# Optimization experiments

Hardware: AMD Instinct MI355X
Metric: run time of the kernel (lower is better)

## Reference

```python
import jax, jax.numpy as jnp
import numpy as np
from jax.scipy.special import logsumexp

DIM_RHO = 128
DIM_C = 128
HID_F = 512   # hidden of MLP2 f
HID_F2 = 256  # hidden of MLP f2 (fixed 128->256->128 in source)
B, S, N = 64, 2048, 100000


def setup_inputs() -> dict:
    key = jax.random.key(0)
    ks = jax.random.split(key, 16)
    def lin(k, fan_in, fan_out):
        bound = 1.0 / np.sqrt(fan_in)
        kw, kb = jax.random.split(k)
        W = jax.random.uniform(kw, (fan_in, fan_out), jnp.float32, -bound, bound)
        b = jax.random.uniform(kb, (fan_out,), jnp.float32, -bound, bound)
        return W, b
    rho = jax.random.normal(ks[0], (B, S, DIM_RHO), jnp.float32)
    c = jax.random.normal(ks[1], (N, DIM_C), jnp.float32)
    w = jax.random.uniform(ks[2], (B, S), jnp.float32, 0.1, 1.0)
    l = jax.random.uniform(ks[3], (B,), jnp.float32, 0.1, 1.0)
    roads = jax.random.randint(ks[4], (B, S), 0, N + 1)  # 0 = pad row
    f2_W1, f2_b1 = lin(ks[5], DIM_C, HID_F2)
    f2_W2, f2_b2 = lin(ks[6], HID_F2, DIM_C)
    f_W1, f_b1 = lin(ks[7], DIM_RHO + DIM_C, HID_F)
    f_W21, f_b21 = lin(ks[8], HID_F, 1)
    f_W22, f_b22 = lin(ks[9], HID_F, 1)
    return {"rho": rho, "c": c, "w": w, "l": l, "roads": roads,
            "f2_W1": f2_W1, "f2_b1": f2_b1, "f2_W2": f2_W2, "f2_b2": f2_b2,
            "f_W1": f_W1, "f_b1": f_b1, "f_W21": f_W21, "f_b21": f_b21,
            "f_W22": f_W22, "f_b22": f_b22}


def reference(rho, c, w, l, roads, f2_W1, f2_b1, f2_W2, f2_b2,
              f_W1, f_b1, f_W21, f_b21, f_W22, f_b22):
    # pad row 0 with zeros, gather per-edge node features: (B, S, dim_c)
    c_padded = jnp.concatenate([jnp.zeros((1, c.shape[1]), c.dtype), c], axis=0)
    c_stack = c_padded[roads]
    # f2: MLP with SELU (dropout inactive at eval)
    h2 = jax.nn.selu(jnp.einsum('bsd,dh->bsh', c_stack, f2_W1) + f2_b1)
    c_t = jnp.einsum('bsh,hd->bsd', h2, f2_W2) + f2_b2
    # f: MLP2 with ReLU (use_selu=False), two heads
    x = jnp.concatenate([rho, c_t], axis=2)  # (B, S, 256)
    h1 = jax.nn.relu(jnp.einsum('bsd,dh->bsh', x, f_W1) + f_b1)
    logm = (jnp.einsum('bsh,ho->bso', h1, f_W21) + f_b21)[..., 0]  # (B, S)
    logv = (jnp.einsum('bsh,ho->bso', h1, f_W22) + f_b22)[..., 0]
    logw = jnp.log(w)
    logm_agg = logsumexp(logm + logw, axis=1)
    logv_agg = logsumexp(logv + 2.0 * logw, axis=1)
    logl = jnp.log(l)
    log_mu = logl - logm_agg
    log_lam = logl - 3.0 * logm_agg - logv_agg
    return (log_mu, log_lam)
```

## Files before the change

kernel.cpp:

```cpp
#include <hip/hip_runtime.h>
#include <hip/hip_bf16.h>

typedef __attribute__((ext_vector_type(8))) short short8;
typedef __attribute__((ext_vector_type(4))) float f32x4;

__device__ __forceinline__ unsigned short f2bf(float f){
    unsigned u = __float_as_uint(f);
    unsigned r = (u + 0x7FFFu + ((u >> 16) & 1u)) >> 16;
    return (unsigned short)r;
}

__device__ __forceinline__ unsigned swz(unsigned row, unsigned byte_in_row, unsigned stride){
    return (row * stride + byte_in_row) ^ ((row & 7u) << 4);
}

__global__ void prep_weights(const float* __restrict__ W1, const float* __restrict__ W2,
                             const float* __restrict__ W3,
                             unsigned short* __restrict__ W1T,
                             unsigned short* __restrict__ W2T,
                             unsigned short* __restrict__ W3T){
    int i = blockIdx.x * 256 + threadIdx.x;
    if (i < 32768){
        int n = i >> 7, k = i & 127;
        W1T[i] = f2bf(W1[k * 256 + n]);
    } else if (i < 65536){
        int j = i - 32768; int n = j >> 8, k = j & 255;
        W2T[j] = f2bf(W2[k * 128 + n]);
    } else if (i < 196608){
        int j = i - 65536; int n = j >> 8, k = j & 255;
        W3T[j] = f2bf(W3[k * 512 + n]);
    }
}

__launch_bounds__(256, 2)
__global__ void main_kernel(const float* __restrict__ rho,
                            const float* __restrict__ c,
                            const float* __restrict__ w,
                            const int*  __restrict__ roads,
                            const unsigned short* __restrict__ W1T,
                            const float* __restrict__ b1,
                            const unsigned short* __restrict__ W2T,
                            const float* __restrict__ b2,
                            const unsigned short* __restrict__ W3T,
                            const float* __restrict__ b3,
                            const float* __restrict__ w21,
                            const float* __restrict__ b21s,
                            const float* __restrict__ w22,
                            const float* __restrict__ b22s,
                            float* __restrict__ pm,
                            float* __restrict__ pv)
{
    __shared__ __align__(16) unsigned char smem[81920];
    unsigned char* sXc = smem;
    unsigned char* sH2 = smem + 16384;
    unsigned char* sX  = smem + 49152;
    float* sPm = (float*)smem;
    float* sPv = (float*)(smem + 4096);

    const int tid = threadIdx.x;
    const int t0  = blockIdx.x * 64;

    for (int u = tid; u < 64 * 32; u += 256){
        int row = u >> 5, ch = u & 31;
        int road = roads[t0 + row];
        float4 v = make_float4(0.f, 0.f, 0.f, 0.f);
        if (road > 0)
            v = reinterpret_cast<const float4*>(c + (size_t)(road - 1) * 128)[ch];
        ushort4 h;
        h.x = f2bf(v.x); h.y = f2bf(v.y); h.z = f2bf(v.z); h.w = f2bf(v.w);
        *reinterpret_cast<ushort4*>(sXc + swz(row, ch * 8, 256)) = h;

        float4 rv = reinterpret_cast<const float4*>(rho + (size_t)(t0 + row) * 128)[ch];
        ushort4 rh;
        rh.x = f2bf(rv.x); rh.y = f2bf(rv.y); rh.z = f2bf(rv.z); rh.w = f2bf(rv.w);
        *reinterpret_cast<ushort4*>(sX + swz(row, ch * 8, 512)) = rh;
    }
    __syncthreads();

    const int lane = tid & 63, wv = tid >> 6;
    const int lr = lane & 15, lg = lane >> 4;

    #pragma unroll
    for (int nc = 0; nc < 4; ++nc){
        const int n = wv * 64 + nc * 16 + lr;
        short8 b[4];
        #pragma unroll
        for (int kk = 0; kk < 4; ++kk)
            b[kk] = *reinterpret_cast<const short8*>(W1T + n * 128 + kk * 32 + lg * 8);
        f32x4 acc[4] = {{0.f,0.f,0.f,0.f},{0.f,0.f,0.f,0.f},{0.f,0.f,0.f,0.f},{0.f,0.f,0.f,0.f}};
        #pragma unroll
        for (int kk = 0; kk < 4; ++kk){
            #pragma unroll
            for (int mt = 0; mt < 4; ++mt){
                short8 a = *reinterpret_cast<const short8*>(sXc + swz(mt * 16 + lr, kk * 64 + lg * 16, 256));
                acc[mt] = __builtin_amdgcn_mfma_f32_16x16x32_bf16(a, b[kk], acc[mt], 0, 0, 0);
            }
        }
        float bias = b1[n];
        #pragma unroll
        for (int mt = 0; mt < 4; ++mt){
            #pragma unroll
            for (int r = 0; r < 4; ++r){
                float vv = acc[mt][r] + bias;
                vv = (vv > 0.f) ? 1.0507009873554805f * vv
                                : 1.7580993408473766f * expm1f(vv);
                *reinterpret_cast<unsigned short*>(sH2 + swz(mt * 16 + lg * 4 + r, n * 2, 512)) = f2bf(vv);
            }
        }
    }
    __syncthreads();

    #pragma unroll
    for (int nc = 0; nc < 2; ++nc){
        const int n = wv * 32 + nc * 16 + lr;
        short8 b[8];
        #pragma unroll
        for (int kk = 0; kk < 8; ++kk)
            b[kk] = *reinterpret_cast<const short8*>(W2T + n * 256 + kk * 32 + lg * 8);
        f32x4 acc[4] = {{0.f,0.f,0.f,0.f},{0.f,0.f,0.f,0.f},{0.f,0.f,0.f,0.f},{0.f,0.f,0.f,0.f}};
        #pragma unroll
        for (int kk = 0; kk < 8; ++kk){
            #pragma unroll
            for (int mt = 0; mt < 4; ++mt){
                short8 a = *reinterpret_cast<const short8*>(sH2 + swz(mt * 16 + lr, kk * 64 + lg * 16, 512));
                acc[mt] = __builtin_amdgcn_mfma_f32_16x16x32_bf16(a, b[kk], acc[mt], 0, 0, 0);
            }
        }
        float bias = b2[n];
        #pragma unroll
        for (int mt = 0; mt < 4; ++mt){
            #pragma unroll
            for (int r = 0; r < 4; ++r){
                float vv = acc[mt][r] + bias;
                *reinterpret_cast<unsigned short*>(sX + swz(mt * 16 + lg * 4 + r, (128 + n) * 2, 512)) = f2bf(vv);
            }
        }
    }
    __syncthreads();

    float hm[4][4] = {};
    float hv[4][4] = {};
    #pragma unroll 2
    for (int nc = 0; nc < 8; ++nc){
        const int n = wv * 128 + nc * 16 + lr;
        short8 b[8];
        #pragma unroll
        for (int kk = 0; kk < 8; ++kk)
            b[kk] = *reinterpret_cast<const short8*>(W3T + n * 256 + kk * 32 + lg * 8);
        f32x4 acc[4] = {{0.f,0.f,0.f,0.f},{0.f,0.f,0.f,0.f},{0.f,0.f,0.f,0.f},{0.f,0.f,0.f,0.f}};
        #pragma unroll
        for (int kk = 0; kk < 8; ++kk){
            #pragma unroll
            for (int mt = 0; mt < 4; ++mt){
                short8 a = *reinterpret_cast<const short8*>(sX + swz(mt * 16 + lr, kk * 64 + lg * 16, 512));
                acc[mt] = __builtin_amdgcn_mfma_f32_16x16x32_bf16(a, b[kk], acc[mt], 0, 0, 0);
            }
        }
        float bias = b3[n];
        float wm = w21[n], wvv = w22[n];
        #pragma unroll
        for (int mt = 0; mt < 4; ++mt){
            #pragma unroll
            for (int r = 0; r < 4; ++r){
                float h = fmaxf(acc[mt][r] + bias, 0.f);
                hm[mt][r] += h * wm;
                hv[mt][r] += h * wvv;
            }
        }
    }
    #pragma unroll
    for (int off = 1; off < 16; off <<= 1){
        #pragma unroll
        for (int mt = 0; mt < 4; ++mt){
            #pragma unroll
            for (int r = 0; r < 4; ++r){
                hm[mt][r] += __shfl_xor(hm[mt][r], off, 64);
                hv[mt][r] += __shfl_xor(hv[mt][r], off, 64);
            }
        }
    }
    if (lr == 0){
        #pragma unroll
        for (int mt = 0; mt < 4; ++mt){
            #pragma unroll
            for (int r = 0; r < 4; ++r){
                int row = mt * 16 + lg * 4 + r;
                sPm[wv * 64 + row] = hm[mt][r];
                sPv[wv * 64 + row] = hv[mt][r];
            }
        }
    }
    __syncthreads();
    if (tid < 64){
        float B21 = b21s[0], B22 = b22s[0];
        float m_ = sPm[tid] + sPm[64 + tid] + sPm[128 + tid] + sPm[192 + tid] + B21;
        float v_ = sPv[tid] + sPv[64 + tid] + sPv[128 + tid] + sPv[192 + tid] + B22;
        int t = t0 + tid;
        float lw = logf(w[t]);
        pm[t] = m_ + lw;
        pv[t] = v_ + 2.f * lw;
    }
}

__global__ void reduce_kernel(const float* __restrict__ pm, const float* __restrict__ pv,
                              const float* __restrict__ l, float* __restrict__ out){
    int b = blockIdx.x;
    int tid = threadIdx.x;
    const float* Pm = pm + (size_t)b * 2048;
    const float* Pv = pv + (size_t)b * 2048;

    float mm = -1e30f, mv = -1e30f;
    for (int i = tid; i < 2048; i += 256){
        mm = fmaxf(mm, Pm[i]);
        mv = fmaxf(mv, Pv[i]);
    }
    __shared__ float redm[4], redv[4];
    #pragma unroll
    for (int off = 32; off > 0; off >>= 1){
        mm = fmaxf(mm, __shfl_xor(mm, off, 64));
        mv = fmaxf(mv, __shfl_xor(mv, off, 64));
    }
    int wv = tid >> 6;
    if ((tid & 63) == 0){ redm[wv] = mm; redv[wv] = mv; }
    __syncthreads();
    mm = fmaxf(fmaxf(redm[0], redm[1]), fmaxf(redm[2], redm[3]));
    mv = fmaxf(fmaxf(redv[0], redv[1]), fmaxf(redv[2], redv[3]));

    float sm = 0.f, sv = 0.f;
    for (int i = tid; i < 2048; i += 256){
        sm += expf(Pm[i] - mm);
        sv += expf(Pv[i] - mv);
    }
    #pragma unroll
    for (int off = 32; off > 0; off >>= 1){
        sm += __shfl_xor(sm, off, 64);
        sv += __shfl_xor(sv, off, 64);
    }
    __shared__ float red2m[4], red2v[4];
    if ((tid & 63) == 0){ red2m[wv] = sm; red2v[wv] = sv; }
    __syncthreads();
    if (tid == 0){
        sm = red2m[0] + red2m[1] + red2m[2] + red2m[3];
        sv = red2v[0] + red2v[1] + red2v[2] + red2v[3];
        float lsem = mm + logf(sm);
        float lsev = mv + logf(sv);
        float ll = logf(l[b]);
        out[b]      = ll - lsem;
        out[64 + b] = ll - 3.f * lsem - lsev;
    }
}

extern "C" void kernel_launch(void* const* d_in, const int* in_sizes, int n_in,
                              void* d_out, int out_size, void* d_ws, size_t ws_size,
                              hipStream_t stream){
    const float* rho   = (const float*)d_in[0];
    const float* c     = (const float*)d_in[1];
    const float* w     = (const float*)d_in[2];
    const float* l     = (const float*)d_in[3];
    const int*   roads = (const int*)  d_in[4];
    const float* f2_W1 = (const float*)d_in[5];
    const float* f2_b1 = (const float*)d_in[6];
    const float* f2_W2 = (const float*)d_in[7];
    const float* f2_b2 = (const float*)d_in[8];
    const float* f_W1  = (const float*)d_in[9];
    const float* f_b1  = (const float*)d_in[10];
    const float* f_W21 = (const float*)d_in[11];
    const float* f_b21 = (const float*)d_in[12];
    const float* f_W22 = (const float*)d_in[13];
    const float* f_b22 = (const float*)d_in[14];

    unsigned char* ws = (unsigned char*)d_ws;
    unsigned short* W1T = (unsigned short*)(ws);
    unsigned short* W2T = (unsigned short*)(ws + 65536);
    unsigned short* W3T = (unsigned short*)(ws + 131072);
    float* pm = (float*)(ws + 393216);
    float* pv = (float*)(ws + 393216 + 524288);

    prep_weights<<<768, 256, 0, stream>>>(f2_W1, f2_W2, f_W1, W1T, W2T, W3T);
    main_kernel<<<2048, 256, 0, stream>>>(rho, c, w, roads,
                                          W1T, f2_b1, W2T, f2_b2, W3T, f_b1,
                                          f_W21, f_b21, f_W22, f_b22, pm, pv);
    reduce_kernel<<<64, 256, 0, stream>>>(pm, pv, l, (float*)d_out);
}
```

Baseline: 157.2 us.

## Use 8 waves per block with transposed MFMA outputs and vectorized epilogues

Doubles the block to 512 threads so each wave owns a narrower slice of output columns in all three GEMM stages. It swaps the MFMA A/B operands so each lane holds four consecutive columns of one row. That allows float4 bias and head-weight loads and ushort4 LDS stores, and cuts the head reduction to two cross-lane shuffles. SELU now uses __expf(v)-1 instead of expm1f, which is slightly less accurate near zero. The launch bound of (512,4) squeezes the register budget and may cause spills, and the 80KB of LDS per block still caps residency.

```diff
diff --git a/kernel.cpp b/kernel.cpp
--- a/kernel.cpp
+++ b/kernel.cpp
@@ -32,7 +32,7 @@
     }
 }
 
-__launch_bounds__(256, 2)
+__launch_bounds__(512, 4)
 __global__ void main_kernel(const float* __restrict__ rho,
                             const float* __restrict__ c,
                             const float* __restrict__ w,
@@ -55,12 +55,12 @@
     unsigned char* sH2 = smem + 16384;
     unsigned char* sX  = smem + 49152;
     float* sPm = (float*)smem;
-    float* sPv = (float*)(smem + 4096);
+    float* sPv = (float*)(smem + 2048);
 
     const int tid = threadIdx.x;
     const int t0  = blockIdx.x * 64;
 
-    for (int u = tid; u < 64 * 32; u += 256){
+    for (int u = tid; u < 64 * 32; u += 512){
         int row = u >> 5, ch = u & 31;
         int road = roads[t0 + row];
         float4 v = make_float4(0.f, 0.f, 0.f, 0.f);
@@ -81,120 +81,125 @@
     const int lr = lane & 15, lg = lane >> 4;
 
     #pragma unroll
-    for (int nc = 0; nc < 4; ++nc){
-        const int n = wv * 64 + nc * 16 + lr;
+    for (int nc = 0; nc < 2; ++nc){
+        const int n0 = wv * 32 + nc * 16;
         short8 b[4];
         #pragma unroll
         for (int kk = 0; kk < 4; ++kk)
-            b[kk] = *reinterpret_cast<const short8*>(W1T + n * 128 + kk * 32 + lg * 8);
+            b[kk] = *reinterpret_cast<const short8*>(W1T + (n0 + lr) * 128 + kk * 32 + lg * 8);
         f32x4 acc[4] = {{0.f,0.f,0.f,0.f},{0.f,0.f,0.f,0.f},{0.f,0.f,0.f,0.f},{0.f,0.f,0.f,0.f}};
         #pragma unroll
         for (int kk = 0; kk < 4; ++kk){
             #pragma unroll
             for (int mt = 0; mt < 4; ++mt){
                 short8 a = *reinterpret_cast<const short8*>(sXc + swz(mt * 16 + lr, kk * 64 + lg * 16, 256));
-                acc[mt] = __builtin_amdgcn_mfma_f32_16x16x32_bf16(a, b[kk], acc[mt], 0, 0, 0);
-            }
-        }
-        float bias = b1[n];
-        #pragma unroll
-        for (int mt = 0; mt < 4; ++mt){
+                acc[mt] = __builtin_amdgcn_mfma_f32_16x16x32_bf16(b[kk], a, acc[mt], 0, 0, 0);
+            }
+        }
+        float4 bb = *reinterpret_cast<const float4*>(b1 + n0 + lg * 4);
+        float bias[4] = {bb.x, bb.y, bb.z, bb.w};
+        #pragma unroll
+        for (int mt = 0; mt < 4; ++mt){
+            ushort4 h;
             #pragma unroll
             for (int r = 0; r < 4; ++r){
-                float vv = acc[mt][r] + bias;
+                float vv = acc[mt][r] + bias[r];
                 vv = (vv > 0.f) ? 1.0507009873554805f * vv
-                                : 1.7580993408473766f * expm1f(vv);
-                *reinterpret_cast<unsigned short*>(sH2 + swz(mt * 16 + lg * 4 + r, n * 2, 512)) = f2bf(vv);
-            }
-        }
-    }
-    __syncthreads();
-
-    #pragma unroll
-    for (int nc = 0; nc < 2; ++nc){
-        const int n = wv * 32 + nc * 16 + lr;
+                                : 1.7580993408473766f * (__expf(vv) - 1.f);
+                reinterpret_cast<unsigned short*>(&h)[r] = f2bf(vv);
+            }
+            *reinterpret_cast<ushort4*>(sH2 + swz(mt * 16 + lr, (n0 + lg * 4) * 2, 512)) = h;
+        }
+    }
+    __syncthreads();
+
+    {
+        const int n0 = wv * 16;
         short8 b[8];
         #pragma unroll
         for (int kk = 0; kk < 8; ++kk)
-            b[kk] = *reinterpret_cast<const short8*>(W2T + n * 256 + kk * 32 + lg * 8);
+            b[kk] = *reinterpret_cast<const short8*>(W2T + (n0 + lr) * 256 + kk * 32 + lg * 8);
         f32x4 acc[4] = {{0.f,0.f,0.f,0.f},{0.f,0.f,0.f,0.f},{0.f,0.f,0.f,0.f},{0.f,0.f,0.f,0.f}};
         #pragma unroll
         for (int kk = 0; kk < 8; ++kk){
             #pragma unroll
             for (int mt = 0; mt < 4; ++mt){
                 short8 a = *reinterpret_cast<const short8*>(sH2 + swz(mt * 16 + lr, kk * 64 + lg * 16, 512));
-                acc[mt] = __builtin_amdgcn_mfma_f32_16x16x32_bf16(a, b[kk], acc[mt], 0, 0, 0);
-            }
-        }
-        float bias = b2[n];
-        #pragma unroll
-        for (int mt = 0; mt < 4; ++mt){
+                acc[mt] = __builtin_amdgcn_mfma_f32_16x16x32_bf16(b[kk], a, acc[mt], 0, 0, 0);
+            }
+        }
+        float4 bb = *reinterpret_cast<const float4*>(b2 + n0 + lg * 4);
+        float bias[4] = {bb.x, bb.y, bb.z, bb.w};
+        #pragma unroll
+        for (int mt = 0; mt < 4; ++mt){
+            ushort4 h;
             #pragma unroll
             for (int r = 0; r < 4; ++r){
-                float vv = acc[mt][r] + bias;
-                *reinterpret_cast<unsigned short*>(sX + swz(mt * 16 + lg * 4 + r, (128 + n) * 2, 512)) = f2bf(vv);
-            }
-        }
-    }
-    __syncthreads();
-
-    float hm[4][4] = {};
-    float hv[4][4] = {};
+                float vv = acc[mt][r] + bias[r];
+                reinterpret_cast<unsigned short*>(&h)[r] = f2bf(vv);
+            }
+            *reinterpret_cast<ushort4*>(sX + swz(mt * 16 + lr, 256 + (n0 + lg * 4) * 2, 512)) = h;
+        }
+    }
+    __syncthreads();
+
+    float hm[4] = {0.f, 0.f, 0.f, 0.f};
+    float hv[4] = {0.f, 0.f, 0.f, 0.f};
     #pragma unroll 2
-    for (int nc = 0; nc < 8; ++nc){
-        const int n = wv * 128 + nc * 16 + lr;
+    for (int nc = 0; nc < 4; ++nc){
+        const int n0 = wv * 64 + nc * 16;
         short8 b[8];
         #pragma unroll
         for (int kk = 0; kk < 8; ++kk)
-            b[kk] = *reinterpret_cast<const short8*>(W3T + n * 256 + kk * 32 + lg * 8);
+            b[kk] = *reinterpret_cast<const short8*>(W3T + (n0 + lr) * 256 + kk * 32 + lg * 8);
         f32x4 acc[4] = {{0.f,0.f,0.f,0.f},{0.f,0.f,0.f,0.f},{0.f,0.f,0.f,0.f},{0.f,0.f,0.f,0.f}};
         #pragma unroll
         for (int kk = 0; kk < 8; ++kk){
             #pragma unroll
             for (int mt = 0; mt < 4; ++mt){
                 short8 a = *reinterpret_cast<const short8*>(sX + swz(mt * 16 + lr, kk * 64 + lg * 16, 512));
-                acc[mt] = __builtin_amdgcn_mfma_f32_16x16x32_bf16(a, b[kk], acc[mt], 0, 0, 0);
-            }
-        }
-        float bias = b3[n];
-        float wm = w21[n], wvv = w22[n];
+                acc[mt] = __builtin_amdgcn_mfma_f32_16x16x32_bf16(b[kk], a, acc[mt], 0, 0, 0);
+            }
+        }
+        float4 b3q = *reinterpret_cast<const float4*>(b3  + n0 + lg * 4);
+        float4 wmq = *reinterpret_cast<const float4*>(w21 + n0 + lg * 4);
+        float4 wvq = *reinterpret_cast<const float4*>(w22 + n0 + lg * 4);
+        float bias[4] = {b3q.x, b3q.y, b3q.z, b3q.w};
+        float wm[4]   = {wmq.x, wmq.y, wmq.z, wmq.w};
+        float wq[4]   = {wvq.x, wvq.y, wvq.z, wvq.w};
         #pragma unroll
         for (int mt = 0; mt < 4; ++mt){
             #pragma unroll
             for (int r = 0; r < 4; ++r){
-                float h = fmaxf(acc[mt][r] + bias, 0.f);
-                hm[mt][r] += h * wm;
-                hv[mt][r] += h * wvv;
-            }
-        }
-    }
-    #pragma unroll
-    for (int off = 1; off < 16; off <<= 1){
-        #pragma unroll
-        for (int mt = 0; mt < 4; ++mt){
-            #pragma unroll
-            for (int r = 0; r < 4; ++r){
-                hm[mt][r] += __shfl_xor(hm[mt][r], off, 64);
-                hv[mt][r] += __shfl_xor(hv[mt][r], off, 64);
-            }
-        }
-    }
-    if (lr == 0){
-        #pragma unroll
-        for (int mt = 0; mt < 4; ++mt){
-            #pragma unroll
-            for (int r = 0; r < 4; ++r){
-                int row = mt * 16 + lg * 4 + r;
-                sPm[wv * 64 + row] = hm[mt][r];
-                sPv[wv * 64 + row] = hv[mt][r];
-            }
+                float h = fmaxf(acc[mt][r] + bias[r], 0.f);
+                hm[mt] += h * wm[r];
+                hv[mt] += h * wq[r];
+            }
+        }
+    }
+    #pragma unroll
+    for (int mt = 0; mt < 4; ++mt){
+        hm[mt] += __shfl_xor(hm[mt], 16, 64);
+        hm[mt] += __shfl_xor(hm[mt], 32, 64);
+        hv[mt] += __shfl_xor(hv[mt], 16, 64);
+        hv[mt] += __shfl_xor(hv[mt], 32, 64);
+    }
+    if (lg == 0){
+        #pragma unroll
+        for (int mt = 0; mt < 4; ++mt){
+            sPm[wv * 64 + mt * 16 + lr] = hm[mt];
+            sPv[wv * 64 + mt * 16 + lr] = hv[mt];
         }
     }
     __syncthreads();
     if (tid < 64){
         float B21 = b21s[0], B22 = b22s[0];
-        float m_ = sPm[tid] + sPm[64 + tid] + sPm[128 + tid] + sPm[192 + tid] + B21;
-        float v_ = sPv[tid] + sPv[64 + tid] + sPv[128 + tid] + sPv[192 + tid] + B22;
+        float m_ = B21, v_ = B22;
+        #pragma unroll
+        for (int k = 0; k < 8; ++k){
+            m_ += sPm[k * 64 + tid];
+            v_ += sPv[k * 64 + tid];
+        }
         int t = t0 + tid;
         float lw = logf(w[t]);
         pm[t] = m_ + lw;
@@ -277,7 +282,7 @@
     float* pv = (float*)(ws + 393216 + 524288);
 
     prep_weights<<<768, 256, 0, stream>>>(f2_W1, f2_W2, f_W1, W1T, W2T, W3T);
-    main_kernel<<<2048, 256, 0, stream>>>(rho, c, w, roads,
+    main_kernel<<<2048, 512, 0, stream>>>(rho, c, w, roads,
                                           W1T, f2_b1, W2T, f2_b2, W3T, f_b1,
                                           f_W21, f_b21, f_W22, f_b22, pm, pv);
     reduce_kernel<<<64, 256, 0, stream>>>(pm, pv, l, (float*)d_out);
```

Result: slower. 248.9 us (+58.4%).
